# Optimization experiments

Measured on AMD Instinct MI355X. Metric: run time of the kernel, lower is better.

The kernel has to match this reference:

```python
import jax, jax.numpy as jnp
import numpy as np

# ---- fixed sizes ----
N_IN = 100_000          # total inner nodes
NODES_PER_INNER = 50    # nodes per inner graph
N_OUT = N_IN // NODES_PER_INNER          # 2000 outer nodes (= num inner graphs)
NODES_PER_OUTER = 125   # outer nodes per outer graph
B = N_OUT // NODES_PER_OUTER             # 16 graphs in the batch
DEG = 8
E_IN = N_IN * DEG        # 800_000 inner edges
E_OUT = N_OUT * DEG      # 16_000 outer edges
IN_FEATS = 64
OUT_FEATS = 64
H = 128                  # h_feats = [128]*6
NUM_CLASSES = 10


def _rand_edges(key, n_graphs, nodes_per_graph, edges_per_graph):
    """Random edges that stay inside each graph of a batched graph."""
    k1, k2 = jax.random.split(key)
    src_l = jax.random.randint(k1, (n_graphs, edges_per_graph), 0, nodes_per_graph)
    dst_l = jax.random.randint(k2, (n_graphs, edges_per_graph), 0, nodes_per_graph)
    off = (jnp.arange(n_graphs) * nodes_per_graph)[:, None]
    return ((src_l + off).reshape(-1).astype(jnp.int32),
            (dst_l + off).reshape(-1).astype(jnp.int32))


def setup_inputs() -> dict:
    key = jax.random.key(0)
    ks = jax.random.split(key, 24)
    inner_src, inner_dst = _rand_edges(ks[0], N_OUT, NODES_PER_INNER, E_IN // N_OUT)
    outer_src, outer_dst = _rand_edges(ks[1], B, NODES_PER_OUTER, E_OUT // B)

    def w(k, fan_in, fan_out):
        return jax.random.normal(k, (fan_in, fan_out), jnp.float32) * (1.0 / np.sqrt(fan_in))

    inp = {
        "in_layer_feat": jax.random.normal(ks[2], (N_IN, IN_FEATS), jnp.float32),
        "out_layer_feat": jax.random.normal(ks[3], (N_OUT, OUT_FEATS), jnp.float32),
        "inner_ew": jax.random.uniform(ks[4], (E_IN,), jnp.float32) + 0.5,
        "outer_ew": jax.random.uniform(ks[5], (E_OUT,), jnp.float32) + 0.5,
        "W1": w(ks[6], IN_FEATS, H),        "b1": jnp.zeros((H,), jnp.float32),
        "W2": w(ks[7], H, H),               "b2": jnp.zeros((H,), jnp.float32),
        "W3": w(ks[8], OUT_FEATS + H, H),   "b3": jnp.zeros((H,), jnp.float32),
        "W4": w(ks[9], H, H),               "b4": jnp.zeros((H,), jnp.float32),
        "W5": w(ks[10], H, H),              "b5": jnp.zeros((H,), jnp.float32),
        "W6": w(ks[11], H, H),              "b6": jnp.zeros((H,), jnp.float32),
        "Wc": w(ks[12], H, NUM_CLASSES),    "bc": jnp.zeros((NUM_CLASSES,), jnp.float32),
        "inner_src": inner_src, "inner_dst": inner_dst,
        "outer_src": outer_src, "outer_dst": outer_dst,
        "inner_node_graph": (jnp.arange(N_IN) // NODES_PER_INNER).astype(jnp.int32),
        "outer_node_graph": (jnp.arange(N_OUT) // NODES_PER_OUTER).astype(jnp.int32),
    }
    return inp


def graph_conv(src, dst, ew, x, W, b, n_nodes):
    """DGL GraphConv, norm='both', weighted aggregation, zero-in-degree allowed."""
    ones = jnp.ones(src.shape[0], x.dtype)
    deg_out = jnp.clip(jax.ops.segment_sum(ones, src, num_segments=n_nodes), 1.0)
    deg_in = jnp.clip(jax.ops.segment_sum(ones, dst, num_segments=n_nodes), 1.0)
    xs = x * jax.lax.rsqrt(deg_out)[:, None]                      # src normalization
    msg = xs[src] * ew[:, None]                                   # u_mul_e
    agg = jax.ops.segment_sum(msg, dst, num_segments=n_nodes)     # copy_e -> sum
    agg = agg * jax.lax.rsqrt(deg_in)[:, None]                    # dst normalization
    return agg @ W + b


def mean_nodes(h, node_graph, n_graphs, nodes_per_graph):
    return jax.ops.segment_sum(h, node_graph, num_segments=n_graphs) / nodes_per_graph


def reference(in_layer_feat, out_layer_feat, inner_ew, outer_ew,
              W1, b1, W2, b2, W3, b3, W4, b4, W5, b5, W6, b6, Wc, bc,
              inner_src, inner_dst, outer_src, outer_dst,
              inner_node_graph, outer_node_graph):
    # inner-graph message passing
    h = jax.nn.relu(graph_conv(inner_src, inner_dst, inner_ew, in_layer_feat, W1, b1, N_IN))
    h = jax.nn.relu(graph_conv(inner_src, inner_dst, inner_ew, h, W2, b2, N_IN))
    reduced = mean_nodes(h, inner_node_graph, N_OUT, float(NODES_PER_INNER))  # [N_OUT, H]
    merged = jnp.concatenate([out_layer_feat, reduced], axis=-1)              # [N_OUT, OUT_FEATS+H]
    # outer-graph message passing
    h = jax.nn.relu(graph_conv(outer_src, outer_dst, outer_ew, merged, W3, b3, N_OUT))
    h = jax.nn.relu(graph_conv(outer_src, outer_dst, outer_ew, h, W4, b4, N_OUT))
    h = jax.nn.relu(graph_conv(outer_src, outer_dst, outer_ew, h, W5, b5, N_OUT))
    h = jax.nn.relu(graph_conv(outer_src, outer_dst, outer_ew, h, W6, b6, N_OUT))
    hg = mean_nodes(h, outer_node_graph, B, float(NODES_PER_OUTER))           # [B, H]
    return hg @ Wc + bc                                                       # [B, NUM_CLASSES]
```

## Files before the change

kernel.cpp:

```cpp
#include <hip/hip_runtime.h>

#define NPI 50
#define EPI 400
#define NPO 125
#define EPO 1000
#define N_IN 100000
#define N_OUT 2000
#define NB 16
#define NC 10

typedef _Float16 half_t;
typedef _Float16 f16x8 __attribute__((ext_vector_type(8)));
typedef float f32x4 __attribute__((ext_vector_type(4)));

#define MFMA(a, b, c) __builtin_amdgcn_mfma_f32_16x16x32_f16(a, b, c, 0, 0, 0)

__device__ __forceinline__ f16x8 lds_ldA(const half_t* base, int row, int kelem, int strideB) {
    return *(const f16x8*)((const char*)base + row * strideB + ((kelem * 2) ^ ((row & 7) << 4)));
}
__device__ __forceinline__ void lds_st(half_t* base, int row, int col, int strideB, float v) {
    *(half_t*)((char*)base + row * strideB + ((col * 2) ^ ((row & 7) << 4))) = (half_t)v;
}
__device__ __forceinline__ void lds_sth(half_t* base, int row, int col, int strideB, half_t v) {
    *(half_t*)((char*)base + row * strideB + ((col * 2) ^ ((row & 7) << 4))) = v;
}

__global__ __launch_bounds__(256) void k_prep(
    const float* __restrict__ W1, const float* __restrict__ W2,
    const float* __restrict__ W3, const float* __restrict__ W4,
    const float* __restrict__ W5, const float* __restrict__ W6,
    half_t* __restrict__ WT1, half_t* __restrict__ WT2,
    half_t* __restrict__ WT3, half_t* __restrict__ WT4,
    half_t* __restrict__ WT5, half_t* __restrict__ WT6)
{
    int i = blockIdx.x * 256 + threadIdx.x;
    const float* src; half_t* dst; int K;
    if      (i < 8192)  { src = W1; dst = WT1; K = 64; }
    else if (i < 24576) { src = W2; dst = WT2; K = 128; i -= 8192; }
    else if (i < 49152) { src = W3; dst = WT3; K = 192; i -= 24576; }
    else if (i < 65536) { src = W4; dst = WT4; K = 128; i -= 49152; }
    else if (i < 81920) { src = W5; dst = WT5; K = 128; i -= 65536; }
    else                { src = W6; dst = WT6; K = 128; i -= 81920; }
    int c = i & 127, k = i >> 7;
    dst[c * K + k] = (half_t)src[k * 128 + c];
}

__global__ __launch_bounds__(256) void k_inner_fused(
    const float* __restrict__ X, const float* __restrict__ outfeat,
    const float* __restrict__ ew, const int* __restrict__ esrc,
    const int* __restrict__ edst,
    const half_t* __restrict__ WT1, const float* __restrict__ b1,
    const half_t* __restrict__ WT2, const float* __restrict__ b2,
    half_t* __restrict__ merged)
{
    __shared__ alignas(16) char smem[42496];
    half_t* Ah   = (half_t*)smem;
    half_t* bufP = (half_t*)(smem + 8192);
    half_t* bufQ = (half_t*)(smem + 24576);
    float*  Af   = (float*)(smem + 24576);
    float*  pool = (float*)(smem + 40960);
    float*  rsoS = (float*)(smem + 41472);
    float*  rsiS = (float*)(smem + 41728);
    int*    cO   = (int*)(smem + 41984);
    int*    cI   = (int*)(smem + 42240);

    const int g = blockIdx.x, t = threadIdx.x;
    const int w = t >> 6, l = t & 63, lr = l & 15, lk = l >> 4;
    const int nb = g * NPI, eb = g * EPI;

    if (t < 64) { cO[t] = 0; cI[t] = 0; }
    if (t >= 64 && t < 192) pool[t - 64] = 0.f;
    for (int i = t; i < NPI * 64; i += 256) Af[i] = 0.f;
    __syncthreads();
    for (int e = t; e < EPI; e += 256) {
        int s = esrc[eb + e] - nb, d = edst[eb + e] - nb;
        atomicAdd(&Af[d * 64 + s], ew[eb + e]);
        atomicAdd(&cO[s], 1); atomicAdd(&cI[d], 1);
    }
    __syncthreads();
    if (t < 64) {
        rsoS[t] = rsqrtf((float)max(cO[t], 1));
        rsiS[t] = rsqrtf((float)max(cI[t], 1));
    }
    __syncthreads();
    for (int i = t; i < 64 * 64; i += 256) {
        int d = i >> 6, s = i & 63;
        float v = (d < NPI && s < NPI) ? Af[d * 64 + s] * rsiS[d] * rsoS[s] : 0.f;
        lds_st(Ah, d, s, 128, v);
    }
    for (int i = t; i < 64 * 64; i += 256) {
        int s = i >> 6, f = i & 63;
        float v = (s < NPI) ? X[(size_t)(nb + s) * 64 + f] : 0.f;
        lds_st(bufP, f, s, 128, v);
    }
    __syncthreads();

    {
        f32x4 acc[4] = {};
        const int ar = w * 16 + lr;
        #pragma unroll
        for (int ks = 0; ks < 2; ks++) {
            f16x8 a = lds_ldA(Ah, ar, ks * 32 + lk * 8, 128);
            #pragma unroll
            for (int nt = 0; nt < 4; nt++) {
                f16x8 b = lds_ldA(bufP, nt * 16 + lr, ks * 32 + lk * 8, 128);
                acc[nt] = MFMA(a, b, acc[nt]);
            }
        }
        #pragma unroll
        for (int nt = 0; nt < 4; nt++)
            #pragma unroll
            for (int q = 0; q < 4; q++)
                lds_st(bufQ, w * 16 + lk * 4 + q, nt * 16 + lr, 256, acc[nt][q]);
    }
    __syncthreads();

    {
        f32x4 acc[8] = {};
        const int ar = w * 16 + lr;
        #pragma unroll
        for (int ks = 0; ks < 2; ks++) {
            f16x8 a = lds_ldA(bufQ, ar, ks * 32 + lk * 8, 256);
            #pragma unroll
            for (int nt = 0; nt < 8; nt++) {
                f16x8 b = *(const f16x8*)&WT1[(nt * 16 + lr) * 64 + ks * 32 + lk * 8];
                acc[nt] = MFMA(a, b, acc[nt]);
            }
        }
        #pragma unroll
        for (int nt = 0; nt < 8; nt++) {
            int f = nt * 16 + lr;
            float bb = b1[f];
            #pragma unroll
            for (int q = 0; q < 4; q++)
                lds_st(bufP, f, w * 16 + lk * 4 + q, 128, fmaxf(acc[nt][q] + bb, 0.f));
        }
    }
    __syncthreads();

    {
        f32x4 acc[8] = {};
        const int ar = w * 16 + lr;
        #pragma unroll
        for (int ks = 0; ks < 2; ks++) {
            f16x8 a = lds_ldA(Ah, ar, ks * 32 + lk * 8, 128);
            #pragma unroll
            for (int nt = 0; nt < 8; nt++) {
                f16x8 b = lds_ldA(bufP, nt * 16 + lr, ks * 32 + lk * 8, 128);
                acc[nt] = MFMA(a, b, acc[nt]);
            }
        }
        #pragma unroll
        for (int nt = 0; nt < 8; nt++)
            #pragma unroll
            for (int q = 0; q < 4; q++)
                lds_st(bufQ, w * 16 + lk * 4 + q, nt * 16 + lr, 256, acc[nt][q]);
    }

    {
        f32x4 acc[8] = {};
        const int ar = w * 16 + lr;
        #pragma unroll
        for (int ks = 0; ks < 4; ks++) {
            f16x8 a = lds_ldA(bufQ, ar, ks * 32 + lk * 8, 256);
            #pragma unroll
            for (int nt = 0; nt < 8; nt++) {
                f16x8 b = *(const f16x8*)&WT2[(nt * 16 + lr) * 128 + ks * 32 + lk * 8];
                acc[nt] = MFMA(a, b, acc[nt]);
            }
        }
        #pragma unroll
        for (int nt = 0; nt < 8; nt++) {
            int f = nt * 16 + lr;
            float bb = b2[f];
            float ps = 0.f;
            #pragma unroll
            for (int q = 0; q < 4; q++) {
                int d = w * 16 + lk * 4 + q;
                float v = fmaxf(acc[nt][q] + bb, 0.f);
                ps += (d < NPI) ? v : 0.f;
            }
            ps += __shfl_xor(ps, 16);
            ps += __shfl_xor(ps, 32);
            if (lk == 0) atomicAdd(&pool[f], ps);
        }
    }
    __syncthreads();
    if (t < 64) merged[(size_t)g * 192 + t] = (half_t)outfeat[(size_t)g * 64 + t];
    else if (t < 192) merged[(size_t)g * 192 + t] = (half_t)(pool[t - 64] * (1.f / NPI));
}

__global__ __launch_bounds__(256) void k_adj_out(
    const float* __restrict__ ew, const int* __restrict__ esrc,
    const int* __restrict__ edst, half_t* __restrict__ Aout)
{
    __shared__ float Af[NPO * NPO];
    __shared__ int cO[NPO], cI[NPO];
    __shared__ float rso[NPO], rsi[NPO];
    const int g = blockIdx.x, t = threadIdx.x;
    const int nb = g * NPO, eb = g * EPO;
    for (int i = t; i < NPO * NPO; i += 256) Af[i] = 0.f;
    if (t < NPO) { cO[t] = 0; cI[t] = 0; }
    __syncthreads();
    for (int e = t; e < EPO; e += 256) {
        int s = esrc[eb + e] - nb, d = edst[eb + e] - nb;
        atomicAdd(&Af[d * NPO + s], ew[eb + e]);
        atomicAdd(&cO[s], 1); atomicAdd(&cI[d], 1);
    }
    __syncthreads();
    if (t < NPO) {
        rso[t] = rsqrtf((float)max(cO[t], 1));
        rsi[t] = rsqrtf((float)max(cI[t], 1));
    }
    __syncthreads();
    for (int i = t; i < 128 * 16; i += 256) {
        int d = i >> 4, s0 = (i & 15) * 8;
        f16x8 v;
        #pragma unroll
        for (int j = 0; j < 8; j++) {
            int s = s0 + j;
            float x = (d < NPO && s < NPO) ? Af[d * NPO + s] * rsi[d] * rso[s] : 0.f;
            v[j] = (half_t)x;
        }
        *(f16x8*)&Aout[(size_t)g * 16384 + d * 128 + s0] = v;
    }
}

template <int FIN, bool STAGE, bool LAST>
__device__ __forceinline__ void outer_layer(
    const half_t* __restrict__ Ag, const half_t* __restrict__ merged_g,
    const half_t* __restrict__ WT, const float* __restrict__ bias,
    half_t* bufP, half_t* bufQ, float* pool,
    int w, int lr, int lk, int t)
{
    f32x4 hacc[2][8] = {};
    constexpr int NCH = FIN / 64;
    #pragma unroll
    for (int ch = 0; ch < NCH; ch++) {
        if constexpr (STAGE) {
            __syncthreads();
            for (int i = t; i < 1024; i += 256) {
                int s = i >> 3, fo = (i & 7) * 8;
                if (s < NPO) {
                    f16x8 hv = *(const f16x8*)&merged_g[(size_t)s * 192 + ch * 64 + fo];
                    #pragma unroll
                    for (int j = 0; j < 8; j++) lds_sth(bufP, fo + j, s, 256, hv[j]);
                } else {
                    #pragma unroll
                    for (int j = 0; j < 8; j++) lds_sth(bufP, fo + j, s, 256, (half_t)0.f);
                }
            }
            __syncthreads();
        }
        const int rowbase = STAGE ? 0 : ch * 64;
        f32x4 tacc[2][4] = {};
        #pragma unroll
        for (int ks = 0; ks < 4; ks++) {
            f16x8 a0 = *(const f16x8*)&Ag[(w * 32 + lr) * 128 + ks * 32 + lk * 8];
            f16x8 a1 = *(const f16x8*)&Ag[(w * 32 + 16 + lr) * 128 + ks * 32 + lk * 8];
            #pragma unroll
            for (int nt = 0; nt < 4; nt++) {
                f16x8 b = lds_ldA(bufP, rowbase + nt * 16 + lr, ks * 32 + lk * 8, 256);
                tacc[0][nt] = MFMA(a0, b, tacc[0][nt]);
                tacc[1][nt] = MFMA(a1, b, tacc[1][nt]);
            }
        }
        #pragma unroll
        for (int rt = 0; rt < 2; rt++)
            #pragma unroll
            for (int nt = 0; nt < 4; nt++)
                #pragma unroll
                for (int q = 0; q < 4; q++)
                    lds_st(bufQ, w * 32 + rt * 16 + lk * 4 + q, nt * 16 + lr, 128,
                           tacc[rt][nt][q]);
        #pragma unroll
        for (int ks = 0; ks < 2; ks++) {
            f16x8 a0 = lds_ldA(bufQ, w * 32 + lr, ks * 32 + lk * 8, 128);
            f16x8 a1 = lds_ldA(bufQ, w * 32 + 16 + lr, ks * 32 + lk * 8, 128);
            #pragma unroll
            for (int nt = 0; nt < 8; nt++) {
                f16x8 b = *(const f16x8*)&WT[(nt * 16 + lr) * FIN + ch * 64 + ks * 32 + lk * 8];
                hacc[0][nt] = MFMA(a0, b, hacc[0][nt]);
                hacc[1][nt] = MFMA(a1, b, hacc[1][nt]);
            }
        }
    }
    __syncthreads();
    if constexpr (!LAST) {
        #pragma unroll
        for (int nt = 0; nt < 8; nt++) {
            int c = nt * 16 + lr;
            float bb = bias[c];
            #pragma unroll
            for (int rt = 0; rt < 2; rt++)
                #pragma unroll
                for (int q = 0; q < 4; q++) {
                    int d = w * 32 + rt * 16 + lk * 4 + q;
                    lds_st(bufP, c, d, 256, fmaxf(hacc[rt][nt][q] + bb, 0.f));
                }
        }
        __syncthreads();
    } else {
        #pragma unroll
        for (int nt = 0; nt < 8; nt++) {
            int c = nt * 16 + lr;
            float bb = bias[c];
            float ps = 0.f;
            #pragma unroll
            for (int rt = 0; rt < 2; rt++)
                #pragma unroll
                for (int q = 0; q < 4; q++) {
                    int d = w * 32 + rt * 16 + lk * 4 + q;
                    float v = fmaxf(hacc[rt][nt][q] + bb, 0.f);
                    ps += (d < NPO) ? v : 0.f;
                }
            ps += __shfl_xor(ps, 16);
            ps += __shfl_xor(ps, 32);
            if (lk == 0) atomicAdd(&pool[c], ps);
        }
        __syncthreads();
    }
}

__global__ __launch_bounds__(256) void k_outer_fused(
    const half_t* __restrict__ Aout, const half_t* __restrict__ merged,
    const half_t* __restrict__ WT3, const float* __restrict__ b3,
    const half_t* __restrict__ WT4, const float* __restrict__ b4,
    const half_t* __restrict__ WT5, const float* __restrict__ b5,
    const half_t* __restrict__ WT6, const float* __restrict__ b6,
    const float* __restrict__ Wc, const float* __restrict__ bc,
    float* __restrict__ out)
{
    __shared__ alignas(16) char smem[49664];
    half_t* bufP = (half_t*)smem;
    half_t* bufQ = (half_t*)(smem + 32768);
    float*  pool = (float*)(smem + 49152);

    const int g = blockIdx.x, t = threadIdx.x;
    const int w = t >> 6, l = t & 63, lr = l & 15, lk = l >> 4;
    const half_t* Ag = Aout + (size_t)g * 16384;
    const half_t* mg = merged + (size_t)g * NPO * 192;

    if (t < 128) pool[t] = 0.f;
    __syncthreads();

    outer_layer<192, true,  false>(Ag, mg, WT3, b3, bufP, bufQ, pool, w, lr, lk, t);
    outer_layer<128, false, false>(Ag, nullptr, WT4, b4, bufP, bufQ, pool, w, lr, lk, t);
    outer_layer<128, false, false>(Ag, nullptr, WT5, b5, bufP, bufQ, pool, w, lr, lk, t);
    outer_layer<128, false, true >(Ag, nullptr, WT6, b6, bufP, bufQ, pool, w, lr, lk, t);

    if (t < NC) {
        float acc = bc[t];
        for (int k = 0; k < 128; k++)
            acc = fmaf(pool[k] * (1.f / NPO), Wc[k * NC + t], acc);
        out[g * NC + t] = acc;
    }
}

extern "C" void kernel_launch(void* const* d_in, const int* in_sizes, int n_in,
                              void* d_out, int out_size, void* d_ws, size_t ws_size,
                              hipStream_t stream)
{
    const float* X       = (const float*)d_in[0];
    const float* outfeat = (const float*)d_in[1];
    const float* iew     = (const float*)d_in[2];
    const float* oew     = (const float*)d_in[3];
    const float* W1 = (const float*)d_in[4];  const float* b1 = (const float*)d_in[5];
    const float* W2 = (const float*)d_in[6];  const float* b2 = (const float*)d_in[7];
    const float* W3 = (const float*)d_in[8];  const float* b3 = (const float*)d_in[9];
    const float* W4 = (const float*)d_in[10]; const float* b4 = (const float*)d_in[11];
    const float* W5 = (const float*)d_in[12]; const float* b5 = (const float*)d_in[13];
    const float* W6 = (const float*)d_in[14]; const float* b6 = (const float*)d_in[15];
    const float* Wc = (const float*)d_in[16]; const float* bc = (const float*)d_in[17];
    const int* isrc = (const int*)d_in[18];   const int* idst = (const int*)d_in[19];
    const int* osrc = (const int*)d_in[20];   const int* odst = (const int*)d_in[21];

    char* base = (char*)d_ws;
    half_t* WT1 = (half_t*)(base + 0);
    half_t* WT2 = (half_t*)(base + 16384);
    half_t* WT3 = (half_t*)(base + 49152);
    half_t* WT4 = (half_t*)(base + 98304);
    half_t* WT5 = (half_t*)(base + 131072);
    half_t* WT6 = (half_t*)(base + 163840);
    half_t* AoutG  = (half_t*)(base + 196608);
    half_t* merged = (half_t*)(base + 720896);

    k_prep<<<384, 256, 0, stream>>>(W1, W2, W3, W4, W5, W6, WT1, WT2, WT3, WT4, WT5, WT6);
    k_adj_out<<<NB, 256, 0, stream>>>(oew, osrc, odst, AoutG);
    k_inner_fused<<<N_OUT, 256, 0, stream>>>(X, outfeat, iew, isrc, idst,
                                             WT1, b1, WT2, b2, merged);
    k_outer_fused<<<NB, 256, 0, stream>>>(AoutG, merged, WT3, b3, WT4, b4,
                                          WT5, b5, WT6, b6, Wc, bc, (float*)d_out);
}
```

Measured before the change: 141.7 us.

## Merge prep kernels, slim inner-kernel LDS, widen outer kernel to 512 threads

Merges the weight-transpose and outer-adjacency kernels into one launch, removing one kernel launch. The inner kernel is restructured to interleave the aggregation and weight GEMMs through a per-wave scratch buffer, which cuts LDS use to raise occupancy (launch bounds 5). It also prefetches edges and features into registers early. The outer kernel now uses 512 threads with one 16-row tile per wave and stages the adjacency in LDS instead of reading it from global memory each layer. The risks are extra recomputation of the A·X tiles per weight-chunk and larger LDS use in the outer kernel.

```diff
diff --git a/kernel.cpp b/kernel.cpp
--- a/kernel.cpp
+++ b/kernel.cpp
@@ -15,37 +15,84 @@
 
 #define MFMA(a, b, c) __builtin_amdgcn_mfma_f32_16x16x32_f16(a, b, c, 0, 0, 0)
 
-__device__ __forceinline__ f16x8 lds_ldA(const half_t* base, int row, int kelem, int strideB) {
-    return *(const f16x8*)((const char*)base + row * strideB + ((kelem * 2) ^ ((row & 7) << 4)));
-}
-__device__ __forceinline__ void lds_st(half_t* base, int row, int col, int strideB, float v) {
+__device__ __forceinline__ f16x8 lds_ld8(const half_t* base, int row, int k, int strideB) {
+    return *(const f16x8*)((const char*)base + row * strideB + ((k * 2) ^ ((row & 7) << 4)));
+}
+__device__ __forceinline__ void lds_st1(half_t* base, int row, int col, int strideB, float v) {
     *(half_t*)((char*)base + row * strideB + ((col * 2) ^ ((row & 7) << 4))) = (half_t)v;
 }
-__device__ __forceinline__ void lds_sth(half_t* base, int row, int col, int strideB, half_t v) {
+__device__ __forceinline__ void lds_st1h(half_t* base, int row, int col, int strideB, half_t v) {
     *(half_t*)((char*)base + row * strideB + ((col * 2) ^ ((row & 7) << 4))) = v;
 }
-
-__global__ __launch_bounds__(256) void k_prep(
+__device__ __forceinline__ void lds_st8(half_t* base, int row, int k, int strideB, f16x8 v) {
+    *(f16x8*)((char*)base + row * strideB + ((k * 2) ^ ((row & 7) << 4))) = v;
+}
+__device__ __forceinline__ f16x8 scr_ld8(const half_t* base, int row, int k) {
+    return *(const f16x8*)((const char*)base + row * 64 + ((k * 2) ^ ((row & 3) << 4)));
+}
+__device__ __forceinline__ void scr_st1(half_t* base, int row, int col, float v) {
+    *(half_t*)((char*)base + row * 64 + ((col * 2) ^ ((row & 3) << 4))) = (half_t)v;
+}
+
+__global__ __launch_bounds__(256) void k_pre(
     const float* __restrict__ W1, const float* __restrict__ W2,
     const float* __restrict__ W3, const float* __restrict__ W4,
     const float* __restrict__ W5, const float* __restrict__ W6,
     half_t* __restrict__ WT1, half_t* __restrict__ WT2,
     half_t* __restrict__ WT3, half_t* __restrict__ WT4,
-    half_t* __restrict__ WT5, half_t* __restrict__ WT6)
-{
-    int i = blockIdx.x * 256 + threadIdx.x;
-    const float* src; half_t* dst; int K;
-    if      (i < 8192)  { src = W1; dst = WT1; K = 64; }
-    else if (i < 24576) { src = W2; dst = WT2; K = 128; i -= 8192; }
-    else if (i < 49152) { src = W3; dst = WT3; K = 192; i -= 24576; }
-    else if (i < 65536) { src = W4; dst = WT4; K = 128; i -= 49152; }
-    else if (i < 81920) { src = W5; dst = WT5; K = 128; i -= 65536; }
-    else                { src = W6; dst = WT6; K = 128; i -= 81920; }
-    int c = i & 127, k = i >> 7;
-    dst[c * K + k] = (half_t)src[k * 128 + c];
-}
-
-__global__ __launch_bounds__(256) void k_inner_fused(
+    half_t* __restrict__ WT5, half_t* __restrict__ WT6,
+    const float* __restrict__ ew, const int* __restrict__ esrc,
+    const int* __restrict__ edst, half_t* __restrict__ Aout)
+{
+    __shared__ float Af[NPO * NPO];
+    __shared__ int cO[NPO], cI[NPO];
+    __shared__ float rso[NPO], rsi[NPO];
+    const int t = threadIdx.x;
+
+    if (blockIdx.x < 384) {
+        int i = blockIdx.x * 256 + t;
+        const float* src; half_t* dst; int K;
+        if      (i < 8192)  { src = W1; dst = WT1; K = 64; }
+        else if (i < 24576) { src = W2; dst = WT2; K = 128; i -= 8192; }
+        else if (i < 49152) { src = W3; dst = WT3; K = 192; i -= 24576; }
+        else if (i < 65536) { src = W4; dst = WT4; K = 128; i -= 49152; }
+        else if (i < 81920) { src = W5; dst = WT5; K = 128; i -= 65536; }
+        else                { src = W6; dst = WT6; K = 128; i -= 81920; }
+        int c = i & 127, k = i >> 7;
+        dst[c * K + k] = (half_t)src[k * 128 + c];
+        return;
+    }
+
+    const int g = blockIdx.x - 384;
+    const int nb = g * NPO, eb = g * EPO;
+    for (int i = t; i < NPO * NPO; i += 256) Af[i] = 0.f;
+    if (t < NPO) { cO[t] = 0; cI[t] = 0; }
+    __syncthreads();
+    for (int e = t; e < EPO; e += 256) {
+        int s = esrc[eb + e] - nb, d = edst[eb + e] - nb;
+        atomicAdd(&Af[d * NPO + s], ew[eb + e]);
+        atomicAdd(&cO[s], 1); atomicAdd(&cI[d], 1);
+    }
+    __syncthreads();
+    if (t < NPO) {
+        rso[t] = rsqrtf((float)max(cO[t], 1));
+        rsi[t] = rsqrtf((float)max(cI[t], 1));
+    }
+    __syncthreads();
+    for (int i = t; i < 128 * 16; i += 256) {
+        int d = i >> 4, s0 = (i & 15) * 8;
+        f16x8 v;
+        #pragma unroll
+        for (int j = 0; j < 8; j++) {
+            int s = s0 + j;
+            float x = (d < NPO && s < NPO) ? Af[d * NPO + s] * rsi[d] * rso[s] : 0.f;
+            v[j] = (half_t)x;
+        }
+        *(f16x8*)&Aout[(size_t)g * 16384 + d * 128 + s0] = v;
+    }
+}
+
+__global__ __launch_bounds__(256, 5) void k_inner(
     const float* __restrict__ X, const float* __restrict__ outfeat,
     const float* __restrict__ ew, const int* __restrict__ esrc,
     const int* __restrict__ edst,
@@ -53,235 +100,187 @@
     const half_t* __restrict__ WT2, const float* __restrict__ b2,
     half_t* __restrict__ merged)
 {
-    __shared__ alignas(16) char smem[42496];
-    half_t* Ah   = (half_t*)smem;
-    half_t* bufP = (half_t*)(smem + 8192);
-    half_t* bufQ = (half_t*)(smem + 24576);
-    float*  Af   = (float*)(smem + 24576);
-    float*  pool = (float*)(smem + 40960);
-    float*  rsoS = (float*)(smem + 41472);
-    float*  rsiS = (float*)(smem + 41728);
-    int*    cO   = (int*)(smem + 41984);
-    int*    cI   = (int*)(smem + 42240);
+    __shared__ alignas(16) char smem[29696];
+    half_t* Ah  = (half_t*)smem;
+    half_t* R2  = (half_t*)(smem + 8192);
+    float*  Af  = (float*)(smem + 8192);
+    half_t* scr = (half_t*)(smem + 24576);
+    float*  pool= (float*)(smem + 28672);
+    int*    cO  = (int*)(smem + 29184);
+    int*    cI  = (int*)(smem + 29440);
 
     const int g = blockIdx.x, t = threadIdx.x;
     const int w = t >> 6, l = t & 63, lr = l & 15, lk = l >> 4;
     const int nb = g * NPI, eb = g * EPI;
+    half_t* scrw = scr + w * 512;
+
+    float ofv = (t < 64) ? outfeat[(size_t)g * 64 + t] : 0.f;
+    int s0e, d0e; float w0e;
+    { int e = eb + t; s0e = esrc[e] - nb; d0e = edst[e] - nb; w0e = ew[e]; }
+    int s1e = 0, d1e = 0; float w1e = 0.f;
+    const bool e1v = (t + 256 < EPI);
+    if (e1v) { int e = eb + t + 256; s1e = esrc[e] - nb; d1e = edst[e] - nb; w1e = ew[e]; }
 
     if (t < 64) { cO[t] = 0; cI[t] = 0; }
     if (t >= 64 && t < 192) pool[t - 64] = 0.f;
-    for (int i = t; i < NPI * 64; i += 256) Af[i] = 0.f;
-    __syncthreads();
-    for (int e = t; e < EPI; e += 256) {
-        int s = esrc[eb + e] - nb, d = edst[eb + e] - nb;
-        atomicAdd(&Af[d * 64 + s], ew[eb + e]);
-        atomicAdd(&cO[s], 1); atomicAdd(&cI[d], 1);
-    }
-    __syncthreads();
-    if (t < 64) {
-        rsoS[t] = rsqrtf((float)max(cO[t], 1));
-        rsiS[t] = rsqrtf((float)max(cI[t], 1));
-    }
-    __syncthreads();
-    for (int i = t; i < 64 * 64; i += 256) {
+    for (int i = t; i < 4096; i += 256) Af[i] = 0.f;
+    __syncthreads();
+
+    atomicAdd(&Af[d0e * 64 + s0e], w0e);
+    atomicAdd(&cO[s0e], 1); atomicAdd(&cI[d0e], 1);
+    if (e1v) {
+        atomicAdd(&Af[d1e * 64 + s1e], w1e);
+        atomicAdd(&cO[s1e], 1); atomicAdd(&cI[d1e], 1);
+    }
+    __syncthreads();
+
+    const int srow = t >> 2, qc = t & 3;
+    float4 xr0 = {0,0,0,0}, xr1 = xr0, xr2 = xr0, xr3 = xr0;
+    if (srow < NPI) {
+        const float* xp = &X[(size_t)(nb + srow) * 64 + qc * 16];
+        xr0 = *(const float4*)(xp + 0);
+        xr1 = *(const float4*)(xp + 4);
+        xr2 = *(const float4*)(xp + 8);
+        xr3 = *(const float4*)(xp + 12);
+    }
+
+    for (int i = t; i < 4096; i += 256) {
         int d = i >> 6, s = i & 63;
-        float v = (d < NPI && s < NPI) ? Af[d * 64 + s] * rsiS[d] * rsoS[s] : 0.f;
-        lds_st(Ah, d, s, 128, v);
-    }
-    for (int i = t; i < 64 * 64; i += 256) {
-        int s = i >> 6, f = i & 63;
-        float v = (s < NPI) ? X[(size_t)(nb + s) * 64 + f] : 0.f;
-        lds_st(bufP, f, s, 128, v);
+        float v = Af[i] * rsqrtf((float)max(cI[d], 1)) * rsqrtf((float)max(cO[s], 1));
+        lds_st1(Ah, d, s, 128, v);
     }
     __syncthreads();
 
     {
-        f32x4 acc[4] = {};
-        const int ar = w * 16 + lr;
-        #pragma unroll
-        for (int ks = 0; ks < 2; ks++) {
-            f16x8 a = lds_ldA(Ah, ar, ks * 32 + lk * 8, 128);
-            #pragma unroll
-            for (int nt = 0; nt < 4; nt++) {
-                f16x8 b = lds_ldA(bufP, nt * 16 + lr, ks * 32 + lk * 8, 128);
-                acc[nt] = MFMA(a, b, acc[nt]);
-            }
-        }
-        #pragma unroll
-        for (int nt = 0; nt < 4; nt++)
-            #pragma unroll
-            for (int q = 0; q < 4; q++)
-                lds_st(bufQ, w * 16 + lk * 4 + q, nt * 16 + lr, 256, acc[nt][q]);
-    }
-    __syncthreads();
-
-    {
-        f32x4 acc[8] = {};
-        const int ar = w * 16 + lr;
-        #pragma unroll
-        for (int ks = 0; ks < 2; ks++) {
-            f16x8 a = lds_ldA(bufQ, ar, ks * 32 + lk * 8, 256);
-            #pragma unroll
-            for (int nt = 0; nt < 8; nt++) {
-                f16x8 b = *(const f16x8*)&WT1[(nt * 16 + lr) * 64 + ks * 32 + lk * 8];
-                acc[nt] = MFMA(a, b, acc[nt]);
-            }
-        }
+        float xv[16] = {xr0.x,xr0.y,xr0.z,xr0.w, xr1.x,xr1.y,xr1.z,xr1.w,
+                        xr2.x,xr2.y,xr2.z,xr2.w, xr3.x,xr3.y,xr3.z,xr3.w};
+        #pragma unroll
+        for (int i = 0; i < 16; i++) lds_st1(R2, qc * 16 + i, srow, 128, xv[i]);
+    }
+    __syncthreads();
+
+    f32x4 hacc[8] = {};
+    #pragma unroll
+    for (int kf = 0; kf < 2; kf++) {
+        #pragma unroll
+        for (int j = 0; j < 2; j++) {
+            const int ft = kf * 2 + j;
+            f32x4 tacc = {};
+            #pragma unroll
+            for (int ks = 0; ks < 2; ks++) {
+                f16x8 a = lds_ld8(Ah, w * 16 + lr, ks * 32 + lk * 8, 128);
+                f16x8 b = lds_ld8(R2, ft * 16 + lr, ks * 32 + lk * 8, 128);
+                tacc = MFMA(a, b, tacc);
+            }
+            #pragma unroll
+            for (int q = 0; q < 4; q++) scr_st1(scrw, lk * 4 + q, j * 16 + lr, tacc[q]);
+        }
+        f16x8 a1 = scr_ld8(scrw, lr, lk * 8);
         #pragma unroll
         for (int nt = 0; nt < 8; nt++) {
-            int f = nt * 16 + lr;
-            float bb = b1[f];
-            #pragma unroll
-            for (int q = 0; q < 4; q++)
-                lds_st(bufP, f, w * 16 + lk * 4 + q, 128, fmaxf(acc[nt][q] + bb, 0.f));
-        }
-    }
-    __syncthreads();
-
-    {
-        f32x4 acc[8] = {};
-        const int ar = w * 16 + lr;
-        #pragma unroll
-        for (int ks = 0; ks < 2; ks++) {
-            f16x8 a = lds_ldA(Ah, ar, ks * 32 + lk * 8, 128);
-            #pragma unroll
-            for (int nt = 0; nt < 8; nt++) {
-                f16x8 b = lds_ldA(bufP, nt * 16 + lr, ks * 32 + lk * 8, 128);
-                acc[nt] = MFMA(a, b, acc[nt]);
-            }
-        }
-        #pragma unroll
-        for (int nt = 0; nt < 8; nt++)
-            #pragma unroll
-            for (int q = 0; q < 4; q++)
-                lds_st(bufQ, w * 16 + lk * 4 + q, nt * 16 + lr, 256, acc[nt][q]);
-    }
-
-    {
-        f32x4 acc[8] = {};
-        const int ar = w * 16 + lr;
-        #pragma unroll
-        for (int ks = 0; ks < 4; ks++) {
-            f16x8 a = lds_ldA(bufQ, ar, ks * 32 + lk * 8, 256);
-            #pragma unroll
-            for (int nt = 0; nt < 8; nt++) {
-                f16x8 b = *(const f16x8*)&WT2[(nt * 16 + lr) * 128 + ks * 32 + lk * 8];
-                acc[nt] = MFMA(a, b, acc[nt]);
-            }
-        }
+            f16x8 b = *(const f16x8*)&WT1[(nt * 16 + lr) * 64 + kf * 32 + lk * 8];
+            hacc[nt] = MFMA(a1, b, hacc[nt]);
+        }
+    }
+    __syncthreads();
+    #pragma unroll
+    for (int nt = 0; nt < 8; nt++) {
+        int c = nt * 16 + lr;
+        float bb = b1[c];
+        #pragma unroll
+        for (int q = 0; q < 4; q++)
+            lds_st1(R2, c, w * 16 + lk * 4 + q, 128, fmaxf(hacc[nt][q] + bb, 0.f));
+    }
+    __syncthreads();
+
+    f32x4 h2[8] = {};
+    #pragma unroll
+    for (int kf = 0; kf < 4; kf++) {
+        #pragma unroll
+        for (int j = 0; j < 2; j++) {
+            const int ft = kf * 2 + j;
+            f32x4 tacc = {};
+            #pragma unroll
+            for (int ks = 0; ks < 2; ks++) {
+                f16x8 a = lds_ld8(Ah, w * 16 + lr, ks * 32 + lk * 8, 128);
+                f16x8 b = lds_ld8(R2, ft * 16 + lr, ks * 32 + lk * 8, 128);
+                tacc = MFMA(a, b, tacc);
+            }
+            #pragma unroll
+            for (int q = 0; q < 4; q++) scr_st1(scrw, lk * 4 + q, j * 16 + lr, tacc[q]);
+        }
+        f16x8 a1 = scr_ld8(scrw, lr, lk * 8);
         #pragma unroll
         for (int nt = 0; nt < 8; nt++) {
-            int f = nt * 16 + lr;
-            float bb = b2[f];
-            float ps = 0.f;
-            #pragma unroll
-            for (int q = 0; q < 4; q++) {
-                int d = w * 16 + lk * 4 + q;
-                float v = fmaxf(acc[nt][q] + bb, 0.f);
-                ps += (d < NPI) ? v : 0.f;
-            }
-            ps += __shfl_xor(ps, 16);
-            ps += __shfl_xor(ps, 32);
-            if (lk == 0) atomicAdd(&pool[f], ps);
-        }
-    }
-    __syncthreads();
-    if (t < 64) merged[(size_t)g * 192 + t] = (half_t)outfeat[(size_t)g * 64 + t];
+            f16x8 b = *(const f16x8*)&WT2[(nt * 16 + lr) * 128 + kf * 32 + lk * 8];
+            h2[nt] = MFMA(a1, b, h2[nt]);
+        }
+    }
+    #pragma unroll
+    for (int nt = 0; nt < 8; nt++) {
+        int c = nt * 16 + lr;
+        float bb = b2[c];
+        float ps = 0.f;
+        #pragma unroll
+        for (int q = 0; q < 4; q++) {
+            int m = w * 16 + lk * 4 + q;
+            float v = fmaxf(h2[nt][q] + bb, 0.f);
+            ps += (m < NPI) ? v : 0.f;
+        }
+        ps += __shfl_xor(ps, 16);
+        ps += __shfl_xor(ps, 32);
+        if (lk == 0) atomicAdd(&pool[c], ps);
+    }
+    __syncthreads();
+    if (t < 64) merged[(size_t)g * 192 + t] = (half_t)ofv;
     else if (t < 192) merged[(size_t)g * 192 + t] = (half_t)(pool[t - 64] * (1.f / NPI));
-}
-
-__global__ __launch_bounds__(256) void k_adj_out(
-    const float* __restrict__ ew, const int* __restrict__ esrc,
-    const int* __restrict__ edst, half_t* __restrict__ Aout)
-{
-    __shared__ float Af[NPO * NPO];
-    __shared__ int cO[NPO], cI[NPO];
-    __shared__ float rso[NPO], rsi[NPO];
-    const int g = blockIdx.x, t = threadIdx.x;
-    const int nb = g * NPO, eb = g * EPO;
-    for (int i = t; i < NPO * NPO; i += 256) Af[i] = 0.f;
-    if (t < NPO) { cO[t] = 0; cI[t] = 0; }
-    __syncthreads();
-    for (int e = t; e < EPO; e += 256) {
-        int s = esrc[eb + e] - nb, d = edst[eb + e] - nb;
-        atomicAdd(&Af[d * NPO + s], ew[eb + e]);
-        atomicAdd(&cO[s], 1); atomicAdd(&cI[d], 1);
-    }
-    __syncthreads();
-    if (t < NPO) {
-        rso[t] = rsqrtf((float)max(cO[t], 1));
-        rsi[t] = rsqrtf((float)max(cI[t], 1));
-    }
-    __syncthreads();
-    for (int i = t; i < 128 * 16; i += 256) {
-        int d = i >> 4, s0 = (i & 15) * 8;
-        f16x8 v;
-        #pragma unroll
-        for (int j = 0; j < 8; j++) {
-            int s = s0 + j;
-            float x = (d < NPO && s < NPO) ? Af[d * NPO + s] * rsi[d] * rso[s] : 0.f;
-            v[j] = (half_t)x;
-        }
-        *(f16x8*)&Aout[(size_t)g * 16384 + d * 128 + s0] = v;
-    }
 }
 
 template <int FIN, bool STAGE, bool LAST>
 __device__ __forceinline__ void outer_layer(
-    const half_t* __restrict__ Ag, const half_t* __restrict__ merged_g,
+    const half_t* AgL, const half_t* __restrict__ mg,
     const half_t* __restrict__ WT, const float* __restrict__ bias,
     half_t* bufP, half_t* bufQ, float* pool,
     int w, int lr, int lk, int t)
 {
-    f32x4 hacc[2][8] = {};
+    f32x4 hacc[8] = {};
     constexpr int NCH = FIN / 64;
     #pragma unroll
     for (int ch = 0; ch < NCH; ch++) {
         if constexpr (STAGE) {
             __syncthreads();
-            for (int i = t; i < 1024; i += 256) {
+            for (int i = t; i < 1024; i += 512) {
                 int s = i >> 3, fo = (i & 7) * 8;
-                if (s < NPO) {
-                    f16x8 hv = *(const f16x8*)&merged_g[(size_t)s * 192 + ch * 64 + fo];
-                    #pragma unroll
-                    for (int j = 0; j < 8; j++) lds_sth(bufP, fo + j, s, 256, hv[j]);
-                } else {
-                    #pragma unroll
-                    for (int j = 0; j < 8; j++) lds_sth(bufP, fo + j, s, 256, (half_t)0.f);
-                }
+                f16x8 hv = {};
+                if (s < NPO) hv = *(const f16x8*)&mg[(size_t)s * 192 + ch * 64 + fo];
+                #pragma unroll
+                for (int j = 0; j < 8; j++) lds_st1h(bufP, fo + j, s, 256, hv[j]);
             }
             __syncthreads();
         }
-        const int rowbase = STAGE ? 0 : ch * 64;
-        f32x4 tacc[2][4] = {};
+        const int rb = STAGE ? 0 : ch * 64;
+        f32x4 tacc[4] = {};
         #pragma unroll
         for (int ks = 0; ks < 4; ks++) {
-            f16x8 a0 = *(const f16x8*)&Ag[(w * 32 + lr) * 128 + ks * 32 + lk * 8];
-            f16x8 a1 = *(const f16x8*)&Ag[(w * 32 + 16 + lr) * 128 + ks * 32 + lk * 8];
+            f16x8 a = lds_ld8(AgL, w * 16 + lr, ks * 32 + lk * 8, 256);
             #pragma unroll
             for (int nt = 0; nt < 4; nt++) {
-                f16x8 b = lds_ldA(bufP, rowbase + nt * 16 + lr, ks * 32 + lk * 8, 256);
-                tacc[0][nt] = MFMA(a0, b, tacc[0][nt]);
-                tacc[1][nt] = MFMA(a1, b, tacc[1][nt]);
-            }
-        }
-        #pragma unroll
-        for (int rt = 0; rt < 2; rt++)
-            #pragma unroll
-            for (int nt = 0; nt < 4; nt++)
-                #pragma unroll
-                for (int q = 0; q < 4; q++)
-                    lds_st(bufQ, w * 32 + rt * 16 + lk * 4 + q, nt * 16 + lr, 128,
-                           tacc[rt][nt][q]);
-        #pragma unroll
-        for (int ks = 0; ks < 2; ks++) {
-            f16x8 a0 = lds_ldA(bufQ, w * 32 + lr, ks * 32 + lk * 8, 128);
-            f16x8 a1 = lds_ldA(bufQ, w * 32 + 16 + lr, ks * 32 + lk * 8, 128);
+                f16x8 b = lds_ld8(bufP, rb + nt * 16 + lr, ks * 32 + lk * 8, 256);
+                tacc[nt] = MFMA(a, b, tacc[nt]);
+            }
+        }
+        #pragma unroll
+        for (int nt = 0; nt < 4; nt++)
+            #pragma unroll
+            for (int q = 0; q < 4; q++)
+                lds_st1(bufQ, w * 16 + lk * 4 + q, nt * 16 + lr, 128, tacc[nt][q]);
+        #pragma unroll
+        for (int ks2 = 0; ks2 < 2; ks2++) {
+            f16x8 a1 = lds_ld8(bufQ, w * 16 + lr, ks2 * 32 + lk * 8, 128);
             #pragma unroll
             for (int nt = 0; nt < 8; nt++) {
-                f16x8 b = *(const f16x8*)&WT[(nt * 16 + lr) * FIN + ch * 64 + ks * 32 + lk * 8];
-                hacc[0][nt] = MFMA(a0, b, hacc[0][nt]);
-                hacc[1][nt] = MFMA(a1, b, hacc[1][nt]);
+                f16x8 b = *(const f16x8*)&WT[(nt * 16 + lr) * FIN + ch * 64 + ks2 * 32 + lk * 8];
+                hacc[nt] = MFMA(a1, b, hacc[nt]);
             }
         }
     }
@@ -292,12 +291,8 @@
             int c = nt * 16 + lr;
             float bb = bias[c];
             #pragma unroll
-            for (int rt = 0; rt < 2; rt++)
-                #pragma unroll
-                for (int q = 0; q < 4; q++) {
-                    int d = w * 32 + rt * 16 + lk * 4 + q;
-                    lds_st(bufP, c, d, 256, fmaxf(hacc[rt][nt][q] + bb, 0.f));
-                }
+            for (int q = 0; q < 4; q++)
+                lds_st1(bufP, c, w * 16 + lk * 4 + q, 256, fmaxf(hacc[nt][q] + bb, 0.f));
         }
         __syncthreads();
     } else {
@@ -307,13 +302,11 @@
             float bb = bias[c];
             float ps = 0.f;
             #pragma unroll
-            for (int rt = 0; rt < 2; rt++)
-                #pragma unroll
-                for (int q = 0; q < 4; q++) {
-                    int d = w * 32 + rt * 16 + lk * 4 + q;
-                    float v = fmaxf(hacc[rt][nt][q] + bb, 0.f);
-                    ps += (d < NPO) ? v : 0.f;
-                }
+            for (int q = 0; q < 4; q++) {
+                int d = w * 16 + lk * 4 + q;
+                float v = fmaxf(hacc[nt][q] + bb, 0.f);
+                ps += (d < NPO) ? v : 0.f;
+            }
             ps += __shfl_xor(ps, 16);
             ps += __shfl_xor(ps, 32);
             if (lk == 0) atomicAdd(&pool[c], ps);
@@ -322,7 +315,7 @@
     }
 }
 
-__global__ __launch_bounds__(256) void k_outer_fused(
+__global__ __launch_bounds__(512) void k_outer(
     const half_t* __restrict__ Aout, const half_t* __restrict__ merged,
     const half_t* __restrict__ WT3, const float* __restrict__ b3,
     const half_t* __restrict__ WT4, const float* __restrict__ b4,
@@ -331,23 +324,28 @@
     const float* __restrict__ Wc, const float* __restrict__ bc,
     float* __restrict__ out)
 {
-    __shared__ alignas(16) char smem[49664];
-    half_t* bufP = (half_t*)smem;
-    half_t* bufQ = (half_t*)(smem + 32768);
-    float*  pool = (float*)(smem + 49152);
+    __shared__ alignas(16) char smem[82432];
+    half_t* AgL  = (half_t*)smem;
+    half_t* bufP = (half_t*)(smem + 32768);
+    half_t* bufQ = (half_t*)(smem + 65536);
+    float*  pool = (float*)(smem + 81920);
 
     const int g = blockIdx.x, t = threadIdx.x;
     const int w = t >> 6, l = t & 63, lr = l & 15, lk = l >> 4;
-    const half_t* Ag = Aout + (size_t)g * 16384;
     const half_t* mg = merged + (size_t)g * NPO * 192;
 
+    for (int i = t; i < 2048; i += 512) {
+        int row = i >> 4, k0 = (i & 15) * 8;
+        f16x8 v = *(const f16x8*)&Aout[(size_t)g * 16384 + row * 128 + k0];
+        lds_st8(AgL, row, k0, 256, v);
+    }
     if (t < 128) pool[t] = 0.f;
     __syncthreads();
 
-    outer_layer<192, true,  false>(Ag, mg, WT3, b3, bufP, bufQ, pool, w, lr, lk, t);
-    outer_layer<128, false, false>(Ag, nullptr, WT4, b4, bufP, bufQ, pool, w, lr, lk, t);
-    outer_layer<128, false, false>(Ag, nullptr, WT5, b5, bufP, bufQ, pool, w, lr, lk, t);
-    outer_layer<128, false, true >(Ag, nullptr, WT6, b6, bufP, bufQ, pool, w, lr, lk, t);
+    outer_layer<192, true,  false>(AgL, mg, WT3, b3, bufP, bufQ, pool, w, lr, lk, t);
+    outer_layer<128, false, false>(AgL, nullptr, WT4, b4, bufP, bufQ, pool, w, lr, lk, t);
+    outer_layer<128, false, false>(AgL, nullptr, WT5, b5, bufP, bufQ, pool, w, lr, lk, t);
+    outer_layer<128, false, true >(AgL, nullptr, WT6, b6, bufP, bufQ, pool, w, lr, lk, t);
 
     if (t < NC) {
         float acc = bc[t];
@@ -385,10 +383,11 @@
     half_t* AoutG  = (half_t*)(base + 196608);
     half_t* merged = (half_t*)(base + 720896);
 
-    k_prep<<<384, 256, 0, stream>>>(W1, W2, W3, W4, W5, W6, WT1, WT2, WT3, WT4, WT5, WT6);
-    k_adj_out<<<NB, 256, 0, stream>>>(oew, osrc, odst, AoutG);
-    k_inner_fused<<<N_OUT, 256, 0, stream>>>(X, outfeat, iew, isrc, idst,
-                                             WT1, b1, WT2, b2, merged);
-    k_outer_fused<<<NB, 256, 0, stream>>>(AoutG, merged, WT3, b3, WT4, b4,
-                                          WT5, b5, WT6, b6, Wc, bc, (float*)d_out);
-}
+    k_pre<<<400, 256, 0, stream>>>(W1, W2, W3, W4, W5, W6,
+                                   WT1, WT2, WT3, WT4, WT5, WT6,
+                                   oew, osrc, odst, AoutG);
+    k_inner<<<N_OUT, 256, 0, stream>>>(X, outfeat, iew, isrc, idst,
+                                       WT1, b1, WT2, b2, merged);
+    k_outer<<<NB, 512, 0, stream>>>(AoutG, merged, WT3, b3, WT4, b4,
+                                    WT5, b5, WT6, b6, Wc, bc, (float*)d_out);
+}
```

Result: faster. 125.8 us (-11.3%).
